# Kernel optimization log

Measured on AMD Instinct MI355X. Metric: run time of the kernel, lower is better.

Reference implementation:

```python
import jax, jax.numpy as jnp
import numpy as np

EPS = 1e-5  # torch BatchNorm1d default eps


def _batchnorm(x, gamma, beta):
    # training-mode BN: biased batch statistics over the node dim
    mu = x.mean(axis=0)
    var = x.var(axis=0)
    return (x - mu) * jax.lax.rsqrt(var + EPS) * gamma + beta


def setup_inputs() -> dict:
    key = jax.random.key(0)
    ks = jax.random.split(key, 12)
    N, E, D_HI, D_LO, D_EMB, D_HID, D_OUT = 50000, 800000, 512, 16, 128, 128, 10
    return {
        "high_dim_features": jax.random.normal(ks[0], (N, D_HI), jnp.float32),
        "low_dim_features": jax.random.normal(ks[1], (N, D_LO), jnp.float32),
        "edge_index": jax.random.randint(ks[2], (2, E), 0, N, jnp.int32),
        "gamma_bn_high": jnp.ones((D_HI,), jnp.float32),
        "beta_bn_high": jnp.zeros((D_HI,), jnp.float32),
        "W_mlp": jax.random.normal(ks[3], (D_HI, D_EMB), jnp.float32) * (1.0 / np.sqrt(D_HI)),
        "b_mlp": jnp.zeros((D_EMB,), jnp.float32),
        "gamma_mlp": jnp.ones((D_EMB,), jnp.float32),
        "beta_mlp": jnp.zeros((D_EMB,), jnp.float32),
        "W_gcn": jax.random.normal(ks[4], (D_EMB, D_HID), jnp.float32) * (1.0 / np.sqrt(D_EMB)),
        "b_gcn": jnp.zeros((D_HID,), jnp.float32),
        "W_cls": jax.random.normal(ks[5], (D_HID, D_OUT), jnp.float32) * (1.0 / np.sqrt(D_HID)),
        "b_cls": jnp.zeros((D_OUT,), jnp.float32),
    }


def reference(high_dim_features, low_dim_features, edge_index,
              gamma_bn_high, beta_bn_high, W_mlp, b_mlp, gamma_mlp, beta_mlp,
              W_gcn, b_gcn, W_cls, b_cls):
    # bn_high -> MLP (linear, relu, bn)
    x = _batchnorm(high_dim_features, gamma_bn_high, beta_bn_high)
    x = _batchnorm(jax.nn.relu(x @ W_mlp + b_mlp), gamma_mlp, beta_mlp)

    # GCNConv with self-loops and symmetric normalization (PyG defaults)
    N = x.shape[0]
    loops = jnp.arange(N, dtype=edge_index.dtype)
    src = jnp.concatenate([edge_index[0], loops])  # [E+N]
    dst = jnp.concatenate([edge_index[1], loops])
    deg = jax.ops.segment_sum(jnp.ones_like(src, dtype=x.dtype), dst, num_segments=N)
    dinv = jax.lax.rsqrt(deg)  # deg >= 1 thanks to self-loops

    h = x @ W_gcn                                   # [N, hidden]
    coef = (dinv[src] * dinv[dst])[:, None]         # [E+N, 1]
    out = jax.ops.segment_sum(h[src] * coef, dst, num_segments=N) + b_gcn

    out = jax.nn.relu(out)
    # dropout(p=0.1) omitted for a deterministic reference (identity)
    logits = out @ W_cls + b_cls
    return jax.nn.log_softmax(logits, axis=1)  # log(softmax(x)) fused stably
```

## Files before the change

kernel.cpp:

```cpp
#include <hip/hip_runtime.h>
#include <math.h>

#define EPS 1e-5f

typedef short short8 __attribute__((ext_vector_type(8)));
typedef float f32x4 __attribute__((ext_vector_type(4)));
typedef unsigned short u16;
typedef u16 u16x4 __attribute__((ext_vector_type(4)));

__device__ inline u16 f2bf(float f) {
  union { float f; unsigned u; } x; x.f = f;
  return (u16)((x.u + 0x7fffu + ((x.u >> 16) & 1u)) >> 16);
}
__device__ inline float bf2f(u16 h) {
  union { float f; unsigned u; } x; x.u = ((unsigned)h) << 16;
  return x.f;
}

__device__ inline void gload_lds16(const void* g, void* l) {
  __builtin_amdgcn_global_load_lds((const __attribute__((address_space(1))) void*)g,
                                   (__attribute__((address_space(3))) void*)l, 16, 0, 0);
}

__global__ void k_zero2(float* __restrict__ a, int na, float* __restrict__ b, int nb) {
  int i = blockIdx.x * 256 + threadIdx.x;
  if (i < na) a[i] = 0.f;
  else if (i - na < nb) b[i - na] = 0.f;
}

__global__ __launch_bounds__(256)
void k_front(const float* __restrict__ X, int N, float* __restrict__ pS,
             float* __restrict__ pQ, u16* __restrict__ Xb,
             const int* __restrict__ dst, int E, int* __restrict__ deg,
             int nbn, int neb) {
  __shared__ float shs[1024], shq[1024];
  int tid = threadIdx.x;
  if ((int)blockIdx.x < nbn) {
    float sum[4] = {0.f, 0.f, 0.f, 0.f}, sq[4] = {0.f, 0.f, 0.f, 0.f};
    size_t total = (size_t)N * 128;
    size_t stride = (size_t)nbn * 512;
    for (size_t i = (size_t)blockIdx.x * 512 + tid; i < total; i += stride) {
      float4 v0 = ((const float4*)X)[i];
      size_t i2 = i + 256;
      bool ok2 = i2 < total;
      float4 v1;
      if (ok2) v1 = ((const float4*)X)[i2];
      u16x4 h0;
      h0[0] = f2bf(v0.x); h0[1] = f2bf(v0.y); h0[2] = f2bf(v0.z); h0[3] = f2bf(v0.w);
      ((u16x4*)Xb)[i] = h0;
      sum[0] += v0.x; sq[0] += v0.x * v0.x;
      sum[1] += v0.y; sq[1] += v0.y * v0.y;
      sum[2] += v0.z; sq[2] += v0.z * v0.z;
      sum[3] += v0.w; sq[3] += v0.w * v0.w;
      if (ok2) {
        u16x4 h1;
        h1[0] = f2bf(v1.x); h1[1] = f2bf(v1.y); h1[2] = f2bf(v1.z); h1[3] = f2bf(v1.w);
        ((u16x4*)Xb)[i2] = h1;
        sum[0] += v1.x; sq[0] += v1.x * v1.x;
        sum[1] += v1.y; sq[1] += v1.y * v1.y;
        sum[2] += v1.z; sq[2] += v1.z * v1.z;
        sum[3] += v1.w; sq[3] += v1.w * v1.w;
      }
    }
#pragma unroll
    for (int i = 0; i < 4; ++i) { shs[tid * 4 + i] = sum[i]; shq[tid * 4 + i] = sq[i]; }
    __syncthreads();
    if (tid < 128) {
#pragma unroll
      for (int i = 0; i < 4; ++i) {
        pS[(size_t)blockIdx.x * 512 + tid * 4 + i] = shs[tid * 4 + i] + shs[(tid + 128) * 4 + i];
        pQ[(size_t)blockIdx.x * 512 + tid * 4 + i] = shq[tid * 4 + i] + shq[(tid + 128) * 4 + i];
      }
    }
  } else {
    int b = (int)blockIdx.x - nbn;
    for (int e = b * 256 + tid; e < E; e += neb * 256)
      atomicAdd(&deg[dst[e]], 1);
  }
}

__global__ __launch_bounds__(256)
void k_mid1(const float* __restrict__ pS, const float* __restrict__ pQ,
            float* __restrict__ s, float* __restrict__ q, int P, int per,
            const int* __restrict__ deg, int N, int* __restrict__ offs,
            int* __restrict__ bsums, float* __restrict__ dinv, int rb) {
  __shared__ int sh[256];
  int t = threadIdx.x;
  if ((int)blockIdx.x < rb) {
    int p0 = blockIdx.x * per;
    int p1 = p0 + per; if (p1 > P) p1 = P;
    float a0 = 0.f, a1 = 0.f, b0 = 0.f, b1 = 0.f;
    for (int p = p0; p < p1; ++p) {
      a0 += pS[(size_t)p * 512 + t];
      a1 += pS[(size_t)p * 512 + t + 256];
      b0 += pQ[(size_t)p * 512 + t];
      b1 += pQ[(size_t)p * 512 + t + 256];
    }
    atomicAdd(&s[t], a0); atomicAdd(&s[t + 256], a1);
    atomicAdd(&q[t], b0); atomicAdd(&q[t + 256], b1);
  } else {
    int bid = (int)blockIdx.x - rb;
    int i = bid * 256 + t;
    int c = (i < N) ? deg[i] : 0;
    if (i < N) dinv[i] = rsqrtf((float)(c + 1));
    int val = c;
    sh[t] = val;
    __syncthreads();
    for (int off = 1; off < 256; off <<= 1) {
      int add = (t >= off) ? sh[t - off] : 0;
      __syncthreads();
      val += add;
      sh[t] = val;
      __syncthreads();
    }
    if (i < N) offs[i] = val - c;
    if (t == 255) bsums[bid] = val;
  }
}

__global__ __launch_bounds__(256)
void k_mid2(const float* __restrict__ s, const float* __restrict__ q,
            const float* __restrict__ gamma, const float* __restrict__ beta,
            const float* __restrict__ W, const float* __restrict__ b,
            u16* __restrict__ WT, float* __restrict__ bp,
            float invN, int lgK, int wb, int fb, int kPerBlock,
            int* __restrict__ bsums, int nb) {
  __shared__ float sh[256];
  __shared__ int shi[256];
  int K = 1 << lgK;
  int t = threadIdx.x;
  if ((int)blockIdx.x < wb) {
    int idx = blockIdx.x * 256 + t;
    int k = idx & (K - 1);
    float mu = s[k] * invN;
    float var = fmaxf(q[k] * invN - mu * mu, 0.f);
    float a = gamma[k] * rsqrtf(var + EPS);
    WT[idx] = f2bf(a * W[(size_t)k * 128 + (idx >> lgK)]);
  } else if ((int)blockIdx.x < wb + fb) {
    int j = t & 127;
    int ksub = t >> 7;
    int k0 = ((int)blockIdx.x - wb) * kPerBlock;
    float acc = 0.f;
    for (int k = k0 + ksub; k < k0 + kPerBlock; k += 2) {
      float mu = s[k] * invN;
      float var = fmaxf(q[k] * invN - mu * mu, 0.f);
      float a = gamma[k] * rsqrtf(var + EPS);
      float c = beta[k] - mu * a;
      acc = fmaf(c, W[(size_t)k * 128 + j], acc);
    }
    sh[t] = acc;
    __syncthreads();
    if (t < 128) {
      float v = sh[t] + sh[t + 128];
      if ((int)blockIdx.x == wb) v += (b ? b[j] : 0.f);
      atomicAdd(&bp[j], v);
    }
  } else {
    if (bsums == nullptr) return;
    int v = (t < nb) ? bsums[t] : 0;
    int val = v;
    shi[t] = val;
    __syncthreads();
    for (int off = 1; off < 256; off <<= 1) {
      int add = (t >= off) ? shi[t - off] : 0;
      __syncthreads();
      val += add;
      shi[t] = val;
      __syncthreads();
    }
    if (t < nb) bsums[t] = val - v;
  }
}

__global__ __launch_bounds__(256)
void k_big(const u16* __restrict__ Xb, const u16* __restrict__ WT,
           const float* __restrict__ bp, u16* __restrict__ Yb,
           float* __restrict__ pS2, float* __restrict__ pQ2, int N,
           const int* __restrict__ src, const int* __restrict__ dst, int E,
           const int* __restrict__ offs, const int* __restrict__ bsums,
           int* __restrict__ cursor, int* __restrict__ col, int gb) {
  __shared__ __align__(16) u16 As[128 * 64];
  __shared__ __align__(16) u16 Bs[128 * 64];
  __shared__ float csum[128], cq[128];
  int tid = threadIdx.x;
  if ((int)blockIdx.x >= gb) {
    int e = ((int)blockIdx.x - gb) * 256 + tid;
    if (e < E) {
      int d = dst[e];
      int p = atomicAdd(&cursor[d], 1);
      col[offs[d] + bsums[d >> 8] + p] = src[e];
    }
    return;
  }
  if (tid < 128) { csum[tid] = 0.f; cq[tid] = 0.f; }
  int lane = tid & 63, wid = tid >> 6;
  int wm = wid & 1, wn = wid >> 1;
  int bRow = blockIdx.x * 128;

  f32x4 acc[4][4];
#pragma unroll
  for (int mi = 0; mi < 4; ++mi)
#pragma unroll
    for (int ni = 0; ni < 4; ++ni) acc[mi][ni] = {0.f, 0.f, 0.f, 0.f};

  for (int k0 = 0; k0 < 512; k0 += 64) {
    __syncthreads();
#pragma unroll
    for (int i = 0; i < 4; ++i) {
      int p = i * 256 + tid;
      int row = p >> 3, slot = p & 7, srs = slot ^ (row & 7);
      int gr = bRow + row; if (gr >= N) gr = N - 1;
      gload_lds16(Xb + (size_t)gr * 512 + (k0 + srs * 8), (char*)As + p * 16);
      gload_lds16(WT + (size_t)row * 512 + (k0 + srs * 8), (char*)Bs + p * 16);
    }
    __syncthreads();
#pragma unroll
    for (int ks = 0; ks < 2; ++ks) {
      short8 af[4], bfv[4];
#pragma unroll
      for (int mi = 0; mi < 4; ++mi) {
        int row = wm * 64 + mi * 16 + (lane & 15);
        int swz = (ks * 4 + (lane >> 4)) ^ (lane & 7);
        af[mi] = *(const short8*)(As + row * 64 + swz * 8);
      }
#pragma unroll
      for (int ni = 0; ni < 4; ++ni) {
        int row = wn * 64 + ni * 16 + (lane & 15);
        int swz = (ks * 4 + (lane >> 4)) ^ (lane & 7);
        bfv[ni] = *(const short8*)(Bs + row * 64 + swz * 8);
      }
#pragma unroll
      for (int mi = 0; mi < 4; ++mi)
#pragma unroll
        for (int ni = 0; ni < 4; ++ni)
          acc[mi][ni] = __builtin_amdgcn_mfma_f32_16x16x32_bf16(af[mi], bfv[ni], acc[mi][ni], 0, 0, 0);
    }
  }

  float bias[4];
#pragma unroll
  for (int ni = 0; ni < 4; ++ni) bias[ni] = bp[wn * 64 + ni * 16 + (lane & 15)];
  float colp[4] = {0, 0, 0, 0}, colq[4] = {0, 0, 0, 0};
#pragma unroll
  for (int mi = 0; mi < 4; ++mi) {
#pragma unroll
    for (int r = 0; r < 4; ++r) {
      int gr = bRow + wm * 64 + mi * 16 + (lane >> 4) * 4 + r;
      if (gr < N) {
#pragma unroll
        for (int ni = 0; ni < 4; ++ni) {
          float u = fmaxf(acc[mi][ni][r] + bias[ni], 0.f);
          colp[ni] += u;
          colq[ni] += u * u;
          Yb[(size_t)gr * 128 + wn * 64 + ni * 16 + (lane & 15)] = f2bf(u);
        }
      }
    }
  }
#pragma unroll
  for (int ni = 0; ni < 4; ++ni) {
    float a = colp[ni], b = colq[ni];
    a += __shfl_xor(a, 16); a += __shfl_xor(a, 32);
    b += __shfl_xor(b, 16); b += __shfl_xor(b, 32);
    if (lane < 16) {
      atomicAdd(&csum[wn * 64 + ni * 16 + lane], a);
      atomicAdd(&cq[wn * 64 + ni * 16 + lane], b);
    }
  }
  __syncthreads();
  if (tid < 128) {
    pS2[(size_t)blockIdx.x * 128 + tid] = csum[tid];
    pQ2[(size_t)blockIdx.x * 128 + tid] = cq[tid];
  }
}

__global__ __launch_bounds__(256)
void k_agg(const float* __restrict__ pS, const float* __restrict__ pQ,
           float* __restrict__ s, float* __restrict__ q, int NB, int per,
           const u16* __restrict__ Yb, const int* __restrict__ col,
           const int* __restrict__ offs, const int* __restrict__ bsums,
           const int* __restrict__ deg, const float* __restrict__ dinv,
           u16* __restrict__ Ab, float* __restrict__ scoef, int N, int rb) {
  int tid = threadIdx.x;
  if ((int)blockIdx.x < rb) {
    int col_ = tid & 127;
    const float* src = (tid >= 128) ? pQ : pS;
    int p0 = blockIdx.x * per;
    int p1 = p0 + per; if (p1 > NB) p1 = NB;
    float a = 0.f;
    for (int p = p0; p < p1; ++p) a += src[(size_t)p * 128 + col_];
    atomicAdd((tid >= 128) ? &q[col_] : &s[col_], a);
    return;
  }
  int wid = tid >> 6;
  int lane = tid & 63;
  int d = ((int)blockIdx.x - rb) * 4 + wid;
  if (d >= N) return;
  int p = offs[d] + bsums[d >> 8];
  int c = deg[d];
  float dd = dinv[d];
  float ax, ay;
  {
    unsigned v = ((const unsigned*)(Yb + (size_t)d * 128))[lane];
    ax = dd * bf2f((u16)v);
    ay = dd * bf2f((u16)(v >> 16));
  }
  float sw = 0.f;
  for (int base = 0; base < c; base += 64) {
    int rem = c - base;
    if (rem > 64) rem = 64;
    int sidx = 0;
    float w = 0.f;
    if (lane < rem) {
      sidx = col[p + base + lane];
      w = dinv[sidx];
    }
    sw += w;
    int j = 0;
    for (; j + 7 < rem; j += 8) {
      int ss[8]; float ww[8]; unsigned vv[8];
#pragma unroll
      for (int u = 0; u < 8; ++u) { ss[u] = __shfl(sidx, j + u); ww[u] = __shfl(w, j + u); }
#pragma unroll
      for (int u = 0; u < 8; ++u) vv[u] = ((const unsigned*)(Yb + (size_t)ss[u] * 128))[lane];
#pragma unroll
      for (int u = 0; u < 8; ++u) {
        ax = fmaf(ww[u], bf2f((u16)vv[u]), ax);
        ay = fmaf(ww[u], bf2f((u16)(vv[u] >> 16)), ay);
      }
    }
    for (; j + 3 < rem; j += 4) {
      int s0 = __shfl(sidx, j), s1 = __shfl(sidx, j + 1);
      int s2 = __shfl(sidx, j + 2), s3 = __shfl(sidx, j + 3);
      float w0 = __shfl(w, j), w1 = __shfl(w, j + 1);
      float w2 = __shfl(w, j + 2), w3 = __shfl(w, j + 3);
      unsigned v0 = ((const unsigned*)(Yb + (size_t)s0 * 128))[lane];
      unsigned v1 = ((const unsigned*)(Yb + (size_t)s1 * 128))[lane];
      unsigned v2 = ((const unsigned*)(Yb + (size_t)s2 * 128))[lane];
      unsigned v3 = ((const unsigned*)(Yb + (size_t)s3 * 128))[lane];
      ax = fmaf(w0, bf2f((u16)v0), ax); ay = fmaf(w0, bf2f((u16)(v0 >> 16)), ay);
      ax = fmaf(w1, bf2f((u16)v1), ax); ay = fmaf(w1, bf2f((u16)(v1 >> 16)), ay);
      ax = fmaf(w2, bf2f((u16)v2), ax); ay = fmaf(w2, bf2f((u16)(v2 >> 16)), ay);
      ax = fmaf(w3, bf2f((u16)v3), ax); ay = fmaf(w3, bf2f((u16)(v3 >> 16)), ay);
    }
    for (; j < rem; ++j) {
      int sj = __shfl(sidx, j);
      float wj = __shfl(w, j);
      unsigned v = ((const unsigned*)(Yb + (size_t)sj * 128))[lane];
      ax = fmaf(wj, bf2f((u16)v), ax);
      ay = fmaf(wj, bf2f((u16)(v >> 16)), ay);
    }
  }
#pragma unroll
  for (int off = 32; off; off >>= 1) sw += __shfl_xor(sw, off);
  unsigned o = (unsigned)f2bf(ax * dd) | ((unsigned)f2bf(ay * dd) << 16);
  ((unsigned*)(Ab + (size_t)d * 128))[lane] = o;
  if (lane == 0) scoef[d] = dd * (sw + dd);
}

__global__ __launch_bounds__(256)
void k_final(const u16* __restrict__ Ab, const u16* __restrict__ W2T,
             const float* __restrict__ hc, const float* __restrict__ scoef,
             const float* __restrict__ bg, const float* __restrict__ Wcls,
             const float* __restrict__ bcls, float* __restrict__ out, int N) {
  __shared__ __align__(16) char smem[65536];
  __shared__ float WcS[1280];
  __shared__ float hcS[128], bgS[128], bcS[10];
  u16* As = (u16*)smem;
  u16* Bs = (u16*)(smem + 32768);
  u16* Tb = (u16*)smem;
  int tid = threadIdx.x;
  for (int i = tid; i < 1280; i += 256) WcS[i] = Wcls[i];
  if (tid < 128) { hcS[tid] = hc[tid]; bgS[tid] = bg[tid]; }
  if (tid < 10) bcS[tid] = bcls[tid];
  int lane = tid & 63, wid = tid >> 6;
  int wm = wid & 1, wn = wid >> 1;
  int bRow = blockIdx.x * 128;

#pragma unroll
  for (int i = 0; i < 8; ++i) {
    int p = i * 256 + tid;
    int row = p >> 4, slot = p & 15, srs = slot ^ (row & 7);
    int gr = bRow + row; if (gr >= N) gr = N - 1;
    gload_lds16(Ab + (size_t)gr * 128 + srs * 8, (char*)As + p * 16);
    gload_lds16(W2T + (size_t)row * 128 + srs * 8, (char*)Bs + p * 16);
  }
  f32x4 acc[4][4];
#pragma unroll
  for (int mi = 0; mi < 4; ++mi)
#pragma unroll
    for (int ni = 0; ni < 4; ++ni) acc[mi][ni] = {0.f, 0.f, 0.f, 0.f};
  __syncthreads();
#pragma unroll
  for (int ks = 0; ks < 4; ++ks) {
    short8 af[4], bfv[4];
#pragma unroll
    for (int mi = 0; mi < 4; ++mi) {
      int row = wm * 64 + mi * 16 + (lane & 15);
      int swz = (ks * 4 + (lane >> 4)) ^ (lane & 7);
      af[mi] = *(const short8*)(As + row * 128 + swz * 8);
    }
#pragma unroll
    for (int ni = 0; ni < 4; ++ni) {
      int row = wn * 64 + ni * 16 + (lane & 15);
      int swz = (ks * 4 + (lane >> 4)) ^ (lane & 7);
      bfv[ni] = *(const short8*)(Bs + row * 128 + swz * 8);
    }
#pragma unroll
    for (int mi = 0; mi < 4; ++mi)
#pragma unroll
      for (int ni = 0; ni < 4; ++ni)
        acc[mi][ni] = __builtin_amdgcn_mfma_f32_16x16x32_bf16(af[mi], bfv[ni], acc[mi][ni], 0, 0, 0);
  }
  __syncthreads();

  float hcv[4], bgv[4];
#pragma unroll
  for (int ni = 0; ni < 4; ++ni) {
    int n = wn * 64 + ni * 16 + (lane & 15);
    hcv[ni] = hcS[n];
    bgv[ni] = bgS[n];
  }
#pragma unroll
  for (int mi = 0; mi < 4; ++mi) {
#pragma unroll
    for (int r = 0; r < 4; ++r) {
      int m = wm * 64 + mi * 16 + (lane >> 4) * 4 + r;
      int gr = bRow + m;
      float sc = (gr < N) ? scoef[gr] : 0.f;
#pragma unroll
      for (int ni = 0; ni < 4; ++ni) {
        float u = fmaxf(acc[mi][ni][r] + hcv[ni] * sc + bgv[ni], 0.f);
        Tb[m * 136 + wn * 64 + ni * 16 + (lane & 15)] = f2bf(u);
      }
    }
  }
  __syncthreads();

  int r2 = tid >> 1, qd = tid & 1;
  float part[10];
#pragma unroll
  for (int t = 0; t < 10; ++t) part[t] = 0.f;
  for (int jj = 0; jj < 64; ++jj) {
    int j = qd * 64 + jj;
    float a = bf2f(Tb[r2 * 136 + j]);
#pragma unroll
    for (int t = 0; t < 10; ++t) part[t] = fmaf(a, WcS[j * 10 + t], part[t]);
  }
#pragma unroll
  for (int t = 0; t < 10; ++t) part[t] += __shfl_xor(part[t], 1);
  int gr = bRow + r2;
  if (qd == 0 && gr < N) {
    float l[10], m = -1e30f;
#pragma unroll
    for (int t = 0; t < 10; ++t) {
      l[t] = part[t] + bcS[t];
      m = fmaxf(m, l[t]);
    }
    float se = 0.f;
#pragma unroll
    for (int t = 0; t < 10; ++t) se += expf(l[t] - m);
    float lse = m + logf(se);
#pragma unroll
    for (int t = 0; t < 10; ++t) out[(size_t)gr * 10 + t] = l[t] - lse;
  }
}

extern "C" void kernel_launch(void* const* d_in, const int* in_sizes, int n_in,
                              void* d_out, int out_size, void* d_ws, size_t ws_size,
                              hipStream_t stream) {
  const float* X = (const float*)d_in[0];
  const int* ei = (const int*)d_in[2];
  const float* gamma1 = (const float*)d_in[3];
  const float* beta1 = (const float*)d_in[4];
  const float* Wmlp = (const float*)d_in[5];
  const float* bmlp = (const float*)d_in[6];
  const float* gamma2 = (const float*)d_in[7];
  const float* beta2 = (const float*)d_in[8];
  const float* Wgcn = (const float*)d_in[9];
  const float* bgcn = (const float*)d_in[10];
  const float* Wcls = (const float*)d_in[11];
  const float* bcls = (const float*)d_in[12];
  float* out = (float*)d_out;

  const int N = in_sizes[0] / 512;
  const int E = in_sizes[2] / 2;
  const float invN = 1.0f / (float)N;

  char* ws = (char*)d_ws;
  float* s1 = (float*)(ws + 0);
  float* q1 = (float*)(ws + 2048);
  float* s2 = (float*)(ws + 4096);
  float* q2 = (float*)(ws + 4608);
  float* b1p = (float*)(ws + 5120);
  float* hconst = (float*)(ws + 5632);
  u16* W1bT = (u16*)(ws + 8192);
  u16* W2bT = (u16*)(ws + 139264);
  int* bsums = (int*)(ws + 172032);
  int* deg = (int*)(ws + 173056);
  int* cursor = (int*)(ws + 373056);
  int* offs = (int*)(ws + 573056);
  float* dinv = (float*)(ws + 773056);
  float* scoef = (float*)(ws + 973056);
  int* col = (int*)(ws + 1173056);
  u16* Yb = (u16*)(ws + 4373504);
  u16* Ab = (u16*)(ws + 17173504);
  u16* Xb = (u16*)(ws + 29973504);
  float* pS1 = (float*)(ws + 81173504);
  float* pQ1 = (float*)(ws + 85367808);
  float* pS2 = (float*)(ws + 89562112);
  float* pQ2 = (float*)(ws + 89762304);
  (void)ws_size; (void)n_in; (void)out_size;

  const int* esrc = ei;
  const int* edst = ei + E;
  int nb = (N + 255) / 256;
  int eb = (E + 255) / 256;
  int gb = (N + 127) / 128;
  const int NBN = 1280;
  const int NEB = 768;

  k_zero2<<<(1536 + 2 * N + 255) / 256, 256, 0, stream>>>(s1, 1536, (float*)deg, 2 * N);
  k_front<<<NBN + NEB, 256, 0, stream>>>(X, N, pS1, pQ1, Xb, edst, E, deg, NBN, NEB);
  k_mid1<<<16 + nb, 256, 0, stream>>>(pS1, pQ1, s1, q1, NBN, 80, deg, N, offs, bsums, dinv, 16);
  k_mid2<<<272 + 1, 256, 0, stream>>>(s1, q1, gamma1, beta1, Wmlp, bmlp, W1bT, b1p,
                                      invN, 9, 256, 16, 32, bsums, nb);
  k_big<<<gb + eb, 256, 0, stream>>>(Xb, W1bT, b1p, Yb, pS2, pQ2, N,
                                     esrc, edst, E, offs, bsums, cursor, col, gb);
  k_agg<<<8 + (N + 3) / 4, 256, 0, stream>>>(pS2, pQ2, s2, q2, gb, (gb + 7) / 8,
                                             Yb, col, offs, bsums, deg, dinv, Ab, scoef, N, 8);
  k_mid2<<<72, 256, 0, stream>>>(s2, q2, gamma2, beta2, Wgcn, nullptr, W2bT, hconst,
                                 invN, 7, 64, 8, 16, nullptr, 0);
  k_final<<<gb, 256, 0, stream>>>(Ab, W2bT, hconst, scoef, bgcn, Wcls, bcls, out, N);
}
```

Measured before the change: 176.4 us.

## Convert X to bf16 inside GEMM loads and record edge slots during degree count

Removes the bf16 copy of the 50000x512 input that k_front used to write. The GEMM now reads fp32 X directly into registers, converts it to bf16 and stores it into LDS, which saves a 51MB write and a 51MB read. The degree-counting atomic now also saves each edge's slot in the CSR, so the CSR fill writes col without a second atomic pass over a cursor array. The cost is that the GEMM reads twice as many A bytes through synchronous register loads instead of async global-to-LDS loads, and there is an extra epos array to write and read.

New measurement: 167.4 us, median of 2. 1.05x faster.

```diff
diff --git a/kernel.cpp b/kernel.cpp
--- a/kernel.cpp
+++ b/kernel.cpp
@@ -30,9 +30,9 @@
 
 __global__ __launch_bounds__(256)
 void k_front(const float* __restrict__ X, int N, float* __restrict__ pS,
-             float* __restrict__ pQ, u16* __restrict__ Xb,
+             float* __restrict__ pQ,
              const int* __restrict__ dst, int E, int* __restrict__ deg,
-             int nbn, int neb) {
+             int* __restrict__ epos, int nbn, int neb) {
   __shared__ float shs[1024], shq[1024];
   int tid = threadIdx.x;
   if ((int)blockIdx.x < nbn) {
@@ -45,17 +45,11 @@
       bool ok2 = i2 < total;
       float4 v1;
       if (ok2) v1 = ((const float4*)X)[i2];
-      u16x4 h0;
-      h0[0] = f2bf(v0.x); h0[1] = f2bf(v0.y); h0[2] = f2bf(v0.z); h0[3] = f2bf(v0.w);
-      ((u16x4*)Xb)[i] = h0;
       sum[0] += v0.x; sq[0] += v0.x * v0.x;
       sum[1] += v0.y; sq[1] += v0.y * v0.y;
       sum[2] += v0.z; sq[2] += v0.z * v0.z;
       sum[3] += v0.w; sq[3] += v0.w * v0.w;
       if (ok2) {
-        u16x4 h1;
-        h1[0] = f2bf(v1.x); h1[1] = f2bf(v1.y); h1[2] = f2bf(v1.z); h1[3] = f2bf(v1.w);
-        ((u16x4*)Xb)[i2] = h1;
         sum[0] += v1.x; sq[0] += v1.x * v1.x;
         sum[1] += v1.y; sq[1] += v1.y * v1.y;
         sum[2] += v1.z; sq[2] += v1.z * v1.z;
@@ -74,8 +68,10 @@
     }
   } else {
     int b = (int)blockIdx.x - nbn;
-    for (int e = b * 256 + tid; e < E; e += neb * 256)
-      atomicAdd(&deg[dst[e]], 1);
+    for (int e = b * 256 + tid; e < E; e += neb * 256) {
+      int d = dst[e];
+      epos[e] = atomicAdd(&deg[d], 1);
+    }
   }
 }
 
@@ -173,12 +169,12 @@
 }
 
 __global__ __launch_bounds__(256)
-void k_big(const u16* __restrict__ Xb, const u16* __restrict__ WT,
+void k_big(const float* __restrict__ X, const u16* __restrict__ WT,
            const float* __restrict__ bp, u16* __restrict__ Yb,
            float* __restrict__ pS2, float* __restrict__ pQ2, int N,
            const int* __restrict__ src, const int* __restrict__ dst, int E,
            const int* __restrict__ offs, const int* __restrict__ bsums,
-           int* __restrict__ cursor, int* __restrict__ col, int gb) {
+           const int* __restrict__ epos, int* __restrict__ col, int gb) {
   __shared__ __align__(16) u16 As[128 * 64];
   __shared__ __align__(16) u16 Bs[128 * 64];
   __shared__ float csum[128], cq[128];
@@ -187,8 +183,7 @@
     int e = ((int)blockIdx.x - gb) * 256 + tid;
     if (e < E) {
       int d = dst[e];
-      int p = atomicAdd(&cursor[d], 1);
-      col[offs[d] + bsums[d >> 8] + p] = src[e];
+      col[offs[d] + bsums[d >> 8] + epos[e]] = src[e];
     }
     return;
   }
@@ -204,14 +199,31 @@
     for (int ni = 0; ni < 4; ++ni) acc[mi][ni] = {0.f, 0.f, 0.f, 0.f};
 
   for (int k0 = 0; k0 < 512; k0 += 64) {
-    __syncthreads();
+    float4 ar[4][2];
 #pragma unroll
     for (int i = 0; i < 4; ++i) {
       int p = i * 256 + tid;
       int row = p >> 3, slot = p & 7, srs = slot ^ (row & 7);
       int gr = bRow + row; if (gr >= N) gr = N - 1;
-      gload_lds16(Xb + (size_t)gr * 512 + (k0 + srs * 8), (char*)As + p * 16);
+      const float4* g = (const float4*)(X + (size_t)gr * 512 + (k0 + srs * 8));
+      ar[i][0] = g[0];
+      ar[i][1] = g[1];
+    }
+    __syncthreads();
+#pragma unroll
+    for (int i = 0; i < 4; ++i) {
+      int p = i * 256 + tid;
+      int row = p >> 3, slot = p & 7, srs = slot ^ (row & 7);
       gload_lds16(WT + (size_t)row * 512 + (k0 + srs * 8), (char*)Bs + p * 16);
+    }
+#pragma unroll
+    for (int i = 0; i < 4; ++i) {
+      int p = i * 256 + tid;
+      const float* f0 = (const float*)&ar[i][0];
+      short8 v;
+#pragma unroll
+      for (int j = 0; j < 8; ++j) v[j] = (short)f2bf(f0[j]);
+      *(short8*)((char*)As + p * 16) = v;
     }
     __syncthreads();
 #pragma unroll
@@ -498,18 +510,17 @@
   u16* W2bT = (u16*)(ws + 139264);
   int* bsums = (int*)(ws + 172032);
   int* deg = (int*)(ws + 173056);
-  int* cursor = (int*)(ws + 373056);
-  int* offs = (int*)(ws + 573056);
-  float* dinv = (float*)(ws + 773056);
-  float* scoef = (float*)(ws + 973056);
-  int* col = (int*)(ws + 1173056);
-  u16* Yb = (u16*)(ws + 4373504);
-  u16* Ab = (u16*)(ws + 17173504);
-  u16* Xb = (u16*)(ws + 29973504);
-  float* pS1 = (float*)(ws + 81173504);
-  float* pQ1 = (float*)(ws + 85367808);
-  float* pS2 = (float*)(ws + 89562112);
-  float* pQ2 = (float*)(ws + 89762304);
+  int* offs = (int*)(ws + 373056);
+  float* dinv = (float*)(ws + 573056);
+  float* scoef = (float*)(ws + 773056);
+  int* col = (int*)(ws + 973056);
+  int* epos = (int*)(ws + 4173056);
+  u16* Yb = (u16*)(ws + 7373056);
+  u16* Ab = (u16*)(ws + 20173056);
+  float* pS1 = (float*)(ws + 32973056);
+  float* pQ1 = (float*)(ws + 35594496);
+  float* pS2 = (float*)(ws + 38215936);
+  float* pQ2 = (float*)(ws + 38416128);
   (void)ws_size; (void)n_in; (void)out_size;
 
   const int* esrc = ei;
@@ -520,13 +531,13 @@
   const int NBN = 1280;
   const int NEB = 768;
 
-  k_zero2<<<(1536 + 2 * N + 255) / 256, 256, 0, stream>>>(s1, 1536, (float*)deg, 2 * N);
-  k_front<<<NBN + NEB, 256, 0, stream>>>(X, N, pS1, pQ1, Xb, edst, E, deg, NBN, NEB);
+  k_zero2<<<(1536 + N + 255) / 256, 256, 0, stream>>>(s1, 1536, (float*)deg, N);
+  k_front<<<NBN + NEB, 256, 0, stream>>>(X, N, pS1, pQ1, edst, E, deg, epos, NBN, NEB);
   k_mid1<<<16 + nb, 256, 0, stream>>>(pS1, pQ1, s1, q1, NBN, 80, deg, N, offs, bsums, dinv, 16);
   k_mid2<<<272 + 1, 256, 0, stream>>>(s1, q1, gamma1, beta1, Wmlp, bmlp, W1bT, b1p,
                                       invN, 9, 256, 16, 32, bsums, nb);
-  k_big<<<gb + eb, 256, 0, stream>>>(Xb, W1bT, b1p, Yb, pS2, pQ2, N,
-                                     esrc, edst, E, offs, bsums, cursor, col, gb);
+  k_big<<<gb + eb, 256, 0, stream>>>(X, W1bT, b1p, Yb, pS2, pQ2, N,
+                                     esrc, edst, E, offs, bsums, epos, col, gb);
   k_agg<<<8 + (N + 3) / 4, 256, 0, stream>>>(pS2, pQ2, s2, q2, gb, (gb + 7) / 8,
                                              Yb, col, offs, bsums, deg, dinv, Ab, scoef, N, 8);
   k_mid2<<<72, 256, 0, stream>>>(s2, q2, gamma2, beta2, Wgcn, nullptr, W2bT, hconst,
```
